# Kernel tuning notes

Hardware: AMD Instinct MI355X
Metric: run time of the kernel (lower is better)

Reference implementation:

```python
import jax, jax.numpy as jnp
import numpy as np
from jax import lax

DIM = 768
HEADS = 12
SR = 2
HH = 64
WW = 64
B = 2
N = HH * WW
HD = DIM // HEADS  # 64; rpe_ratio=1.0 -> rotary covers full head dim


def _angles(dim, end, W, step=1, bias=0.0, theta=10000.0):
    # 2D rotary angles, interleaved x/y: [end, dim//2]
    flat = jnp.arange(end)
    xp = bias + (flat % W) * step
    yp = bias + (flat // W) * step
    freqs = 1.0 / theta ** (jnp.arange(0, dim, 4)[: dim // 4].astype(jnp.float32) / dim)
    xf = jnp.outer(xp.astype(jnp.float32), freqs)
    yf = jnp.outer(yp.astype(jnp.float32), freqs)
    return jnp.stack([xf, yf], axis=-1).reshape(end, -1)


def _rope(x, ang):
    # x: [B, N, h, d]; ang: [N, d//2]
    x2 = x.reshape(x.shape[:-1] + (-1, 2))
    c = jnp.cos(ang)[None, :, None, :]
    s = jnp.sin(ang)[None, :, None, :]
    x0, x1 = x2[..., 0], x2[..., 1]
    out = jnp.stack([x0 * c - x1 * s, x0 * s + x1 * c], axis=-1)
    return out.reshape(x.shape)


def setup_inputs() -> dict:
    key = jax.random.key(0)
    ks = jax.random.split(key, 6)
    p = lambda k, sh: jax.random.normal(k, sh, dtype=jnp.float32) * 0.02
    return {
        'x': jax.random.normal(ks[0], (B, N, DIM), dtype=jnp.float32),
        'Wq': p(ks[1], (DIM, DIM)),
        'Wkv': p(ks[2], (2 * DIM, DIM)),
        'sr_w': p(ks[3], (DIM, DIM, SR, SR)),
        'sr_b': jnp.zeros((DIM,), jnp.float32),
        'ln_g': jnp.ones((DIM,), jnp.float32),
        'ln_b': jnp.zeros((DIM,), jnp.float32),
        'proj_w': p(ks[4], (DIM, DIM)),
        'proj_b': jnp.zeros((DIM,), jnp.float32),
        'H': HH,
        'W': WW,
    }


def reference(x, Wq, Wkv, sr_w, sr_b, ln_g, ln_b, proj_w, proj_b, H, W):
    Bn, Nn, C = x.shape
    hd = C // HEADS
    scale = hd ** -0.5
    N_red = (H * W) // (SR * SR)

    q = (x @ Wq.T).reshape(Bn, Nn, HEADS, hd)

    # spatial reduction: strided conv + layernorm
    xc = x.transpose(0, 2, 1).reshape(Bn, C, H, W)
    xr = lax.conv_general_dilated(xc, sr_w, (SR, SR), 'VALID',
                                  dimension_numbers=('NCHW', 'OIHW', 'NCHW'))
    xr = xr + sr_b[None, :, None, None]
    xr = xr.reshape(Bn, C, N_red).transpose(0, 2, 1)  # [B, N_red, C]
    mu = xr.mean(-1, keepdims=True)
    var = ((xr - mu) ** 2).mean(-1, keepdims=True)
    xr = (xr - mu) / jnp.sqrt(var + 1e-5) * ln_g + ln_b

    kv = (xr @ Wkv.T).reshape(Bn, N_red, 2, HEADS, hd)
    k, v = kv[:, :, 0], kv[:, :, 1]

    # partial-dim 2D rotary (rpe_dim == head_dim here); k uses step=SR, bias=1-1/SR
    q = _rope(q, _angles(hd, Nn, W))
    k = _rope(k, _angles(hd, N_red, W, step=SR, bias=1.0 - 1.0 / SR))

    attn = jnp.einsum('bnhd,bmhd->bhnm', q, k) * scale

    # custom spatial causal mask
    flat = jnp.arange(H * W)
    xpos = flat // (SR * H)
    ox = flat // H
    oy = flat % H
    ypos = (ox + oy * H) // (SR * H)
    vis = xpos * SR + ypos + 1  # number of visible reduced tokens per query
    mask = jnp.arange(N_red)[None, :] < vis[:, None]  # [N, N_red]
    attn = attn + jnp.where(mask, 0.0, -jnp.inf)[None, None]

    attn = jax.nn.softmax(attn, axis=-1)
    out = jnp.einsum('bhnm,bmhd->bnhd', attn, v).reshape(Bn, Nn, C)
    return out @ proj_w.T + proj_b
```

## Files before the change

### kernel.cpp

```cpp
#include <hip/hip_runtime.h>
#include <hip/hip_bf16.h>
#include <math.h>

typedef __attribute__((ext_vector_type(4))) float f32x4;
typedef __attribute__((ext_vector_type(8))) short short8;
typedef __attribute__((ext_vector_type(8))) unsigned short ushort8;
typedef __attribute__((ext_vector_type(4))) unsigned short ushort4v;

__device__ __forceinline__ unsigned short f2bf(float f) {
  __hip_bfloat16 h = __float2bfloat16(f);
  return *reinterpret_cast<unsigned short*>(&h);
}
__device__ __forceinline__ float bf2f(unsigned short u) {
  unsigned v = ((unsigned)u) << 16;
  return *reinterpret_cast<float*>(&v);
}
__device__ __forceinline__ void async16(const void* g, void* l) {
  __builtin_amdgcn_global_load_lds(
      (__attribute__((address_space(1))) void*)g,
      (__attribute__((address_space(3))) void*)l, 16, 0, 0);
}
#define WAITVM8 { asm volatile("s_waitcnt vmcnt(8)" ::: "memory"); __builtin_amdgcn_sched_barrier(0); }
#define WAITVM4 { asm volatile("s_waitcnt vmcnt(4)" ::: "memory"); __builtin_amdgcn_sched_barrier(0); }
#define WAITVM0 { asm volatile("s_waitcnt vmcnt(0)" ::: "memory"); __builtin_amdgcn_sched_barrier(0); }

__global__ __launch_bounds__(256) void k_prep(
    const float* __restrict__ x, const float* __restrict__ Wq,
    const float* __restrict__ Wkv, const float* __restrict__ pw,
    const float* __restrict__ srw,
    float* __restrict__ qtab, float* __restrict__ ktab,
    unsigned short* __restrict__ xb, unsigned short* __restrict__ wqb,
    unsigned short* __restrict__ wkvb, unsigned short* __restrict__ pwb,
    unsigned short* __restrict__ wsrb)
{
  int idx = blockIdx.x * 256 + threadIdx.x;
  if (idx < 131072) {
    int n = idx >> 5, i = idx & 31;
    float freq = powf(10000.0f, -(float)(i >> 1) * (1.0f / 16.0f));
    float pos = (i & 1) ? (float)(n >> 6) : (float)(n & 63);
    float a = pos * freq;
    qtab[idx * 2] = cosf(a);
    qtab[idx * 2 + 1] = sinf(a);
  } else if (idx < 163840) {
    int t = idx - 131072;
    int m = t >> 5, i = t & 31;
    float freq = powf(10000.0f, -(float)(i >> 1) * (1.0f / 16.0f));
    float pos = (i & 1) ? (0.5f + 2.0f * (float)(m >> 6)) : (0.5f + 2.0f * (float)(m & 63));
    float a = pos * freq;
    ktab[t * 2] = cosf(a);
    ktab[t * 2 + 1] = sinf(a);
  } else if (idx < 1736704) {
    int g = idx - 163840;
    float4 v = ((const float4*)x)[g];
    ushort4v o; o[0]=f2bf(v.x); o[1]=f2bf(v.y); o[2]=f2bf(v.z); o[3]=f2bf(v.w);
    *(ushort4v*)(xb + g * 4) = o;
  } else if (idx < 1884160) {
    int g = idx - 1736704;
    float4 v = ((const float4*)Wq)[g];
    ushort4v o; o[0]=f2bf(v.x); o[1]=f2bf(v.y); o[2]=f2bf(v.z); o[3]=f2bf(v.w);
    *(ushort4v*)(wqb + g * 4) = o;
  } else if (idx < 2179072) {
    int g = idx - 1884160;
    float4 v = ((const float4*)Wkv)[g];
    ushort4v o; o[0]=f2bf(v.x); o[1]=f2bf(v.y); o[2]=f2bf(v.z); o[3]=f2bf(v.w);
    *(ushort4v*)(wkvb + g * 4) = o;
  } else if (idx < 2326528) {
    int g = idx - 2179072;
    float4 v = ((const float4*)pw)[g];
    ushort4v o; o[0]=f2bf(v.x); o[1]=f2bf(v.y); o[2]=f2bf(v.z); o[3]=f2bf(v.w);
    *(ushort4v*)(pwb + g * 4) = o;
  } else if (idx < 4685824) {
    int g = idx - 2326528;
    int o = g / 3072;
    int rem = g - o * 3072;
    int c = rem >> 2, patch = rem & 3;
    wsrb[(size_t)patch * 589824 + o * 768 + c] = f2bf(srw[g]);
  }
}

template<int MODE>
__global__ __launch_bounds__(256) void k_g(
    const unsigned short* __restrict__ A, const unsigned short* __restrict__ W,
    void* __restrict__ O0, void* __restrict__ O1,
    const float* __restrict__ bias, const float* __restrict__ tab)
{
  __shared__ __align__(16) unsigned short As[4][128][32];
  __shared__ __align__(16) unsigned short Ws[4][128][32];
  const int tid = threadIdx.x, lane = tid & 63, wid = tid >> 6;
  const int wr = (wid >> 1) * 64, wc = (wid & 1) * 64;
  const int l15 = lane & 15, lhi = lane >> 4;
  const int K = 768, NT = 24;

  const int NWG = (MODE == 1) ? 192 : 384;
  const int tile = ((int)blockIdx.x & 7) * (NWG >> 3) + ((int)blockIdx.x >> 3);

  int cm, cn, patch = 0;
  if (MODE == 3) {
    patch = tile / 96; int r = tile - patch * 96;
    cm = (r / 6) * 128; cn = (r % 6) * 128;
  } else if (MODE == 1) {
    cm = (tile / 12) * 128; cn = (tile % 12) * 128;
  } else {
    cm = (tile / 6) * 128; cn = (tile % 6) * 128;
  }

  size_t aoff0, aoff1;
  {
    int r0 = cm + wid * 32 + (lane >> 2);
    int r1 = r0 + 16;
    if (MODE == 3) {
      int kh = patch >> 1, kw = patch & 1;
      int b0 = r0 >> 10, p0 = r0 & 1023;
      int b1 = r1 >> 10, p1 = r1 & 1023;
      r0 = b0 * 4096 + (2 * (p0 >> 5) + kh) * 64 + 2 * (p0 & 31) + kw;
      r1 = b1 * 4096 + (2 * (p1 >> 5) + kh) * 64 + 2 * (p1 & 31) + kw;
    }
    aoff0 = (size_t)r0 * K + (lane & 3) * 8;
    aoff1 = (size_t)r1 * K + (lane & 3) * 8;
  }
  const unsigned short* wbase = (MODE == 3) ? (W + (size_t)patch * 589824) : W;
  size_t woff0 = (size_t)(cn + wid * 32 + (lane >> 2)) * K + (lane & 3) * 8;
  size_t woff1 = woff0 + (size_t)16 * K;

#define STAGE(bi, kt) { \
    async16(A + aoff0 + (kt) * 32,     &As[bi][wid * 32][0]);      \
    async16(A + aoff1 + (kt) * 32,     &As[bi][wid * 32 + 16][0]); \
    async16(wbase + woff0 + (kt) * 32, &Ws[bi][wid * 32][0]);      \
    async16(wbase + woff1 + (kt) * 32, &Ws[bi][wid * 32 + 16][0]); }

  f32x4 zero = {0.f, 0.f, 0.f, 0.f};
  f32x4 acc[4][4];
  #pragma unroll
  for (int i = 0; i < 4; i++)
    #pragma unroll
    for (int j = 0; j < 4; j++) acc[i][j] = zero;

  STAGE(0, 0);
  STAGE(1, 1);
  STAGE(2, 2);

  #pragma unroll 4
  for (int kt = 0; kt < NT; ++kt) {
    if (kt + 2 < NT)      WAITVM8
    else if (kt + 1 < NT) WAITVM4
    else                  WAITVM0
    __builtin_amdgcn_s_barrier();
    __builtin_amdgcn_sched_barrier(0);
    const int bi = kt & 3;
    if (kt + 3 < NT) STAGE((kt + 3) & 3, kt + 3);
    short8 af[4], wf[4];
    #pragma unroll
    for (int m = 0; m < 4; m++) af[m] = *(const short8*)&As[bi][wr + m * 16 + l15][lhi * 8];
    #pragma unroll
    for (int n = 0; n < 4; n++) wf[n] = *(const short8*)&Ws[bi][wc + n * 16 + l15][lhi * 8];
    #pragma unroll
    for (int m = 0; m < 4; m++)
      #pragma unroll
      for (int n = 0; n < 4; n++)
        acc[m][n] = __builtin_amdgcn_mfma_f32_16x16x32_bf16(wf[n], af[m], acc[m][n], 0, 0, 0);
  }
#undef STAGE

  if (MODE == 0) {
    float* O = (float*)O0;
    #pragma unroll
    for (int n = 0; n < 4; n++) {
      int colb = cn + wc + n * 16 + lhi * 4;
      f32x4 bv = *(const f32x4*)&bias[colb];
      #pragma unroll
      for (int m = 0; m < 4; m++) {
        int row = cm + wr + m * 16 + l15;
        f32x4 v = acc[m][n] + bv;
        *(f32x4*)&O[(size_t)row * 768 + colb] = v;
      }
    }
  } else if (MODE == 2) {
    unsigned short* qr = (unsigned short*)O0;
    const float2* t2 = (const float2*)tab;
    #pragma unroll
    for (int n = 0; n < 4; n++) {
      int col = cn + wc + n * 16 + lhi * 4;
      int hh = col >> 6, d0 = col & 63, i0 = d0 >> 1;
      #pragma unroll
      for (int m = 0; m < 4; m++) {
        int row = cm + wr + m * 16 + l15;
        int bb = row >> 12, np = row & 4095;
        float2 cs0 = t2[np * 32 + i0];
        float2 cs1 = t2[np * 32 + i0 + 1];
        f32x4 v = acc[m][n];
        ushort4v o;
        o[0] = f2bf(v[0] * cs0.x - v[1] * cs0.y);
        o[1] = f2bf(v[0] * cs0.y + v[1] * cs0.x);
        o[2] = f2bf(v[2] * cs1.x - v[3] * cs1.y);
        o[3] = f2bf(v[2] * cs1.y + v[3] * cs1.x);
        *(ushort4v*)(qr + ((size_t)(bb * 12 + hh) * 4096 + np) * 64 + d0) = o;
      }
    }
  } else if (MODE == 1) {
    unsigned short* kr = (unsigned short*)O0;
    unsigned short* vr = (unsigned short*)O1;
    const float2* t2 = (const float2*)tab;
    #pragma unroll
    for (int n = 0; n < 4; n++) {
      int col = cn + wc + n * 16 + lhi * 4;
      bool isk = (col < 768);
      int c2 = isk ? col : col - 768;
      int hh = c2 >> 6, d0 = c2 & 63, i0 = d0 >> 1;
      #pragma unroll
      for (int m = 0; m < 4; m++) {
        int row = cm + wr + m * 16 + l15;
        int bb = row >> 10, mm = row & 1023;
        f32x4 v = acc[m][n];
        size_t o = ((size_t)(bb * 12 + hh) * 1024 + mm) * 64 + d0;
        ushort4v pk;
        if (isk) {
          float2 cs0 = t2[mm * 32 + i0];
          float2 cs1 = t2[mm * 32 + i0 + 1];
          pk[0] = f2bf(v[0] * cs0.x - v[1] * cs0.y);
          pk[1] = f2bf(v[0] * cs0.y + v[1] * cs0.x);
          pk[2] = f2bf(v[2] * cs1.x - v[3] * cs1.y);
          pk[3] = f2bf(v[2] * cs1.y + v[3] * cs1.x);
          *(ushort4v*)(kr + o) = pk;
        } else {
          pk[0] = f2bf(v[0]); pk[1] = f2bf(v[1]);
          pk[2] = f2bf(v[2]); pk[3] = f2bf(v[3]);
          *(ushort4v*)(vr + o) = pk;
        }
      }
    }
  } else {
    unsigned short* O = (unsigned short*)O0 + (size_t)patch * 2048 * 768;
    #pragma unroll
    for (int n = 0; n < 4; n++) {
      int colb = cn + wc + n * 16 + lhi * 4;
      #pragma unroll
      for (int m = 0; m < 4; m++) {
        int row = cm + wr + m * 16 + l15;
        f32x4 v = acc[m][n];
        ushort4v pk;
        pk[0] = f2bf(v[0]); pk[1] = f2bf(v[1]);
        pk[2] = f2bf(v[2]); pk[3] = f2bf(v[3]);
        *(ushort4v*)(O + (size_t)row * 768 + colb) = pk;
      }
    }
  }
}

__global__ __launch_bounds__(256) void k_lnr(const unsigned short* __restrict__ part,
    const float* __restrict__ srb, const float* __restrict__ g,
    const float* __restrict__ b, unsigned short* __restrict__ out) {
  int row = blockIdx.x;
  int t = threadIdx.x;
  float v[3];
  #pragma unroll
  for (int j = 0; j < 3; j++) {
    int c = t + j * 256;
    float s = srb[c];
    #pragma unroll
    for (int p = 0; p < 4; p++)
      s += bf2f(part[((size_t)p * 2048 + row) * 768 + c]);
    v[j] = s;
  }
  float s = v[0] + v[1] + v[2];
  float s2 = v[0] * v[0] + v[1] * v[1] + v[2] * v[2];
  #pragma unroll
  for (int off = 1; off < 64; off <<= 1) {
    s += __shfl_xor(s, off);
    s2 += __shfl_xor(s2, off);
  }
  __shared__ float ss[4], ss2[4];
  int w = t >> 6;
  if ((t & 63) == 0) { ss[w] = s; ss2[w] = s2; }
  __syncthreads();
  s = ss[0] + ss[1] + ss[2] + ss[3];
  s2 = ss2[0] + ss2[1] + ss2[2] + ss2[3];
  float mu = s * (1.0f / 768.0f);
  float var = s2 * (1.0f / 768.0f) - mu * mu;
  float rstd = rsqrtf(var + 1e-5f);
  unsigned short* o = out + (size_t)row * 768;
  #pragma unroll
  for (int j = 0; j < 3; j++) {
    int c = t + j * 256;
    o[c] = f2bf((v[j] - mu) * rstd * g[c] + b[c]);
  }
}

__global__ __launch_bounds__(256) void k_attn(
    const unsigned short* __restrict__ qr,
    const unsigned short* __restrict__ kr,
    const unsigned short* __restrict__ vr,
    unsigned short* __restrict__ aout)
{
  __shared__ __align__(16) unsigned short kt_s[96][72];
  __shared__ __align__(16) unsigned short vt_s[64][104];
  __shared__ __align__(16) unsigned short p_s[4][16][104];

  const int qt = blockIdx.x;
  const int h = blockIdx.y;
  const int b = blockIdx.z;
  const int bh = b * 12 + h;
  const int tid = threadIdx.x, lane = tid & 63, w = tid >> 6;
  const int l15 = lane & 15, lhi = lane >> 4;

  const unsigned short* kg = kr + (size_t)bh * 1024 * 64;
  #pragma unroll
  for (int it = 0; it < 3; it++) {
    int ch = it * 256 + tid;
    int row = ch >> 3, c8 = (ch & 7) * 8;
    *(ushort8*)&kt_s[row][c8] = *(const ushort8*)(kg + row * 64 + c8);
  }
  const unsigned short* vg = vr + (size_t)bh * 1024 * 64;
  #pragma unroll
  for (int it = 0; it < 24; it++) {
    int e = it * 256 + tid;
    int row = e >> 6, d = e & 63;
    vt_s[d][row] = vg[row * 64 + d];
  }
  __syncthreads();

  const unsigned short* qg = qr + (size_t)bh * 4096 * 64
                           + (size_t)(qt * 64 + w * 16 + l15) * 64 + lhi * 8;
  short8 qf0 = *(const short8*)qg;
  short8 qf1 = *(const short8*)(qg + 32);

  f32x4 zero = {0.f, 0.f, 0.f, 0.f};
  f32x4 sacc[6];
  #pragma unroll
  for (int g = 0; g < 6; g++) sacc[g] = zero;
  #pragma unroll
  for (int g = 0; g < 6; g++) {
    short8 kf0 = *(const short8*)&kt_s[g * 16 + l15][lhi * 8];
    short8 kf1 = *(const short8*)&kt_s[g * 16 + l15][32 + lhi * 8];
    sacc[g] = __builtin_amdgcn_mfma_f32_16x16x32_bf16(qf0, kf0, sacc[g], 0, 0, 0);
    sacc[g] = __builtin_amdgcn_mfma_f32_16x16x32_bf16(qf1, kf1, sacc[g], 0, 0, 0);
  }

  int visv[4];
  #pragma unroll
  for (int r = 0; r < 4; r++) {
    int n = qt * 64 + w * 16 + lhi * 4 + r;
    visv[r] = 2 * (n >> 7) + (((n >> 6) + ((n & 63) << 6)) >> 7) + 1;
  }

  float mx[4] = {-INFINITY, -INFINITY, -INFINITY, -INFINITY};
  #pragma unroll
  for (int g = 0; g < 6; g++) {
    int key = g * 16 + l15;
    #pragma unroll
    for (int r = 0; r < 4; r++) {
      float s = (key < visv[r]) ? sacc[g][r] * 0.125f : -INFINITY;
      sacc[g][r] = s;
      mx[r] = fmaxf(mx[r], s);
    }
  }
  #pragma unroll
  for (int off = 1; off < 16; off <<= 1) {
    #pragma unroll
    for (int r = 0; r < 4; r++) mx[r] = fmaxf(mx[r], __shfl_xor(mx[r], off));
  }
  float sum[4] = {0.f, 0.f, 0.f, 0.f};
  #pragma unroll
  for (int g = 0; g < 6; g++) {
    #pragma unroll
    for (int r = 0; r < 4; r++) {
      float pv = __expf(sacc[g][r] - mx[r]);
      sum[r] += pv;
      p_s[w][lhi * 4 + r][g * 16 + l15] = f2bf(pv);
    }
  }
  #pragma unroll
  for (int off = 1; off < 16; off <<= 1) {
    #pragma unroll
    for (int r = 0; r < 4; r++) sum[r] += __shfl_xor(sum[r], off);
  }
  __syncthreads();

  f32x4 oacc[4];
  #pragma unroll
  for (int dg = 0; dg < 4; dg++) oacc[dg] = zero;
  #pragma unroll
  for (int ks = 0; ks < 3; ks++) {
    short8 pa = *(const short8*)&p_s[w][l15][ks * 32 + lhi * 8];
    #pragma unroll
    for (int dg = 0; dg < 4; dg++) {
      short8 vb = *(const short8*)&vt_s[dg * 16 + l15][ks * 32 + lhi * 8];
      oacc[dg] = __builtin_amdgcn_mfma_f32_16x16x32_bf16(pa, vb, oacc[dg], 0, 0, 0);
    }
  }

  unsigned short* ob = aout + ((size_t)b * 4096 + qt * 64 + w * 16) * 768 + h * 64;
  #pragma unroll
  for (int dg = 0; dg < 4; dg++) {
    int d = dg * 16 + l15;
    #pragma unroll
    for (int r = 0; r < 4; r++) {
      ob[(size_t)(lhi * 4 + r) * 768 + d] = f2bf(oacc[dg][r] / sum[r]);
    }
  }
}

extern "C" void kernel_launch(void* const* d_in, const int* in_sizes, int n_in,
                              void* d_out, int out_size, void* d_ws, size_t ws_size,
                              hipStream_t stream) {
  const float* x   = (const float*)d_in[0];
  const float* Wq  = (const float*)d_in[1];
  const float* Wkv = (const float*)d_in[2];
  const float* srw = (const float*)d_in[3];
  const float* srb = (const float*)d_in[4];
  const float* lng = (const float*)d_in[5];
  const float* lnb = (const float*)d_in[6];
  const float* pw  = (const float*)d_in[7];
  const float* pb  = (const float*)d_in[8];

  char* ws = (char*)d_ws;
  float* qtab           = (float*)(ws);
  float* ktab           = (float*)(ws + 1048576);
  unsigned short* xb    = (unsigned short*)(ws + 1310720);
  unsigned short* attno = xb;
  unsigned short* qrope = (unsigned short*)(ws + 13893632);
  unsigned short* part  = (unsigned short*)(ws + 26476544);
  unsigned short* kr    = (unsigned short*)(ws + 26476544);
  unsigned short* vr    = (unsigned short*)(ws + 29622272);
  unsigned short* wqb   = (unsigned short*)(ws + 39059456);
  unsigned short* wkvb  = (unsigned short*)(ws + 40239104);
  unsigned short* pwb   = (unsigned short*)(ws + 42598400);
  unsigned short* wsrb  = (unsigned short*)(ws + 43778048);
  unsigned short* xrn   = (unsigned short*)(ws + 48496640);

  k_prep<<<18304, 256, 0, stream>>>(x, Wq, Wkv, pw, srw, qtab, ktab,
                                    xb, wqb, wkvb, pwb, wsrb);
  k_g<2><<<384, 256, 0, stream>>>(xb, wqb, qrope, nullptr, nullptr, qtab);
  k_g<3><<<384, 256, 0, stream>>>(xb, wsrb, part, nullptr, nullptr, nullptr);
  k_lnr<<<2048, 256, 0, stream>>>(part, srb, lng, lnb, xrn);
  k_g<1><<<192, 256, 0, stream>>>(xrn, wkvb, kr, vr, nullptr, ktab);
  k_attn<<<dim3(64, 12, 2), 256, 0, stream>>>(qrope, kr, vr, attno);
  k_g<0><<<384, 256, 0, stream>>>(attno, pwb, d_out, nullptr, pb, nullptr);
}
```

Measured before the change: 127.7 us.

## Pre-tile operands into contiguous K-blocks and fuse Q and conv GEMM launches

Prep now writes x and all weights in a tiled [rowblock][ktile][128][32] bf16 layout, including a separate pre-gathered copy of x for the strided conv patches. Each GEMM stage then loads one contiguous 8 KB block per operand instead of strided rows. The Q projection and the conv reduction run in a single launch, with conv tiles summing two patches over K=1536 so only two partials reach the layernorm. Attention output and layernorm output are also written tiled. In exchange the extra x copy adds write traffic, the conv tiles do twice the K loop (load imbalance), and the tiled stores from attention and layernorm are scattered.

```diff
diff --git a/kernel.cpp b/kernel.cpp
--- a/kernel.cpp
+++ b/kernel.cpp
@@ -23,15 +23,16 @@
 #define WAITVM8 { asm volatile("s_waitcnt vmcnt(8)" ::: "memory"); __builtin_amdgcn_sched_barrier(0); }
 #define WAITVM4 { asm volatile("s_waitcnt vmcnt(4)" ::: "memory"); __builtin_amdgcn_sched_barrier(0); }
 #define WAITVM0 { asm volatile("s_waitcnt vmcnt(0)" ::: "memory"); __builtin_amdgcn_sched_barrier(0); }
+
 
 __global__ __launch_bounds__(256) void k_prep(
     const float* __restrict__ x, const float* __restrict__ Wq,
     const float* __restrict__ Wkv, const float* __restrict__ pw,
     const float* __restrict__ srw,
     float* __restrict__ qtab, float* __restrict__ ktab,
-    unsigned short* __restrict__ xb, unsigned short* __restrict__ wqb,
-    unsigned short* __restrict__ wkvb, unsigned short* __restrict__ pwb,
-    unsigned short* __restrict__ wsrb)
+    unsigned short* __restrict__ xq_t, unsigned short* __restrict__ xc_t,
+    unsigned short* __restrict__ wq_t, unsigned short* __restrict__ wkv_t,
+    unsigned short* __restrict__ pw_t, unsigned short* __restrict__ wsr_t)
 {
   int idx = blockIdx.x * 256 + threadIdx.x;
   if (idx < 131072) {
@@ -49,84 +50,113 @@
     float a = pos * freq;
     ktab[t * 2] = cosf(a);
     ktab[t * 2 + 1] = sinf(a);
-  } else if (idx < 1736704) {
+  } else if (idx < 557056) {
     int g = idx - 163840;
-    float4 v = ((const float4*)x)[g];
-    ushort4v o; o[0]=f2bf(v.x); o[1]=f2bf(v.y); o[2]=f2bf(v.z); o[3]=f2bf(v.w);
-    *(ushort4v*)(xb + g * 4) = o;
-  } else if (idx < 1884160) {
-    int g = idx - 1736704;
-    float4 v = ((const float4*)Wq)[g];
-    ushort4v o; o[0]=f2bf(v.x); o[1]=f2bf(v.y); o[2]=f2bf(v.z); o[3]=f2bf(v.w);
-    *(ushort4v*)(wqb + g * 4) = o;
-  } else if (idx < 2179072) {
-    int g = idx - 1884160;
-    float4 v = ((const float4*)Wkv)[g];
-    ushort4v o; o[0]=f2bf(v.x); o[1]=f2bf(v.y); o[2]=f2bf(v.z); o[3]=f2bf(v.w);
-    *(ushort4v*)(wkvb + g * 4) = o;
-  } else if (idx < 2326528) {
-    int g = idx - 2179072;
-    float4 v = ((const float4*)pw)[g];
-    ushort4v o; o[0]=f2bf(v.x); o[1]=f2bf(v.y); o[2]=f2bf(v.z); o[3]=f2bf(v.w);
-    *(ushort4v*)(pwb + g * 4) = o;
-  } else if (idx < 4685824) {
-    int g = idx - 2326528;
-    int o = g / 3072;
-    int rem = g - o * 3072;
-    int c = rem >> 2, patch = rem & 3;
-    wsrb[(size_t)patch * 589824 + o * 768 + c] = f2bf(srw[g]);
+    int row = g / 48, c16 = g - row * 48;
+    int kt = c16 >> 1, half = (c16 & 1) * 16;
+    const float4* xp = (const float4*)(x + (size_t)row * 768 + c16 * 16);
+    float4 f0 = xp[0], f1 = xp[1], f2 = xp[2], f3 = xp[3];
+    ushort8 u0, u1;
+    u0[0]=f2bf(f0.x); u0[1]=f2bf(f0.y); u0[2]=f2bf(f0.z); u0[3]=f2bf(f0.w);
+    u0[4]=f2bf(f1.x); u0[5]=f2bf(f1.y); u0[6]=f2bf(f1.z); u0[7]=f2bf(f1.w);
+    u1[0]=f2bf(f2.x); u1[1]=f2bf(f2.y); u1[2]=f2bf(f2.z); u1[3]=f2bf(f2.w);
+    u1[4]=f2bf(f3.x); u1[5]=f2bf(f3.y); u1[6]=f2bf(f3.z); u1[7]=f2bf(f3.w);
+    size_t dq = ((size_t)((row >> 7) * 24 + kt) * 128 + (row & 127)) * 32 + half;
+    *(ushort8*)(xq_t + dq) = u0;
+    *(ushort8*)(xq_t + dq + 8) = u1;
+    int rowm = row & 4095, bb = row >> 12;
+    int hh = rowm >> 6, www = rowm & 63;
+    int patch = (hh & 1) * 2 + (www & 1);
+    int convrow = bb * 1024 + (hh >> 1) * 32 + (www >> 1);
+    size_t dc = ((size_t)((patch * 16 + (convrow >> 7)) * 24 + kt) * 128 + (convrow & 127)) * 32 + half;
+    *(ushort8*)(xc_t + dc) = u0;
+    *(ushort8*)(xc_t + dc + 8) = u1;
+  } else if (idx < 851968) {
+    const float* src; unsigned short* dst; int g;
+    if (idx < 593920)      { g = idx - 557056; src = Wq;  dst = wq_t; }
+    else if (idx < 667648) { g = idx - 593920; src = Wkv; dst = wkv_t; }
+    else if (idx < 704512) { g = idx - 667648; src = pw;  dst = pw_t; }
+    else {
+      int t = idx - 704512;
+      int o = t / 192, c4 = t - o * 192, c = c4 * 4;
+      const float4* sp = (const float4*)(srw + (size_t)o * 3072 + c * 4);
+      float4 q0 = sp[0], q1 = sp[1], q2 = sp[2], q3 = sp[3];
+      float qa[4][4] = {{q0.x,q0.y,q0.z,q0.w},{q1.x,q1.y,q1.z,q1.w},
+                        {q2.x,q2.y,q2.z,q2.w},{q3.x,q3.y,q3.z,q3.w}};
+      #pragma unroll
+      for (int p = 0; p < 4; p++) {
+        ushort4v wv;
+        #pragma unroll
+        for (int j = 0; j < 4; j++) wv[j] = f2bf(qa[j][p]);
+        size_t d = ((size_t)((p * 6 + (o >> 7)) * 24 + (c >> 5)) * 128 + (o & 127)) * 32 + (c & 31);
+        *(ushort4v*)(wsr_t + d) = wv;
+      }
+      return;
+    }
+    int row = g / 48, c16 = g - row * 48;
+    int kt = c16 >> 1, half = (c16 & 1) * 16;
+    const float4* xp = (const float4*)(src + (size_t)row * 768 + c16 * 16);
+    float4 f0 = xp[0], f1 = xp[1], f2 = xp[2], f3 = xp[3];
+    ushort8 u0, u1;
+    u0[0]=f2bf(f0.x); u0[1]=f2bf(f0.y); u0[2]=f2bf(f0.z); u0[3]=f2bf(f0.w);
+    u0[4]=f2bf(f1.x); u0[5]=f2bf(f1.y); u0[6]=f2bf(f1.z); u0[7]=f2bf(f1.w);
+    u1[0]=f2bf(f2.x); u1[1]=f2bf(f2.y); u1[2]=f2bf(f2.z); u1[3]=f2bf(f2.w);
+    u1[4]=f2bf(f3.x); u1[5]=f2bf(f3.y); u1[6]=f2bf(f3.z); u1[7]=f2bf(f3.w);
+    size_t d = ((size_t)((row >> 7) * 24 + kt) * 128 + (row & 127)) * 32 + half;
+    *(ushort8*)(dst + d) = u0;
+    *(ushort8*)(dst + d + 8) = u1;
   }
 }
 
 template<int MODE>
 __global__ __launch_bounds__(256) void k_g(
-    const unsigned short* __restrict__ A, const unsigned short* __restrict__ W,
+    const unsigned short* __restrict__ A, const unsigned short* __restrict__ A2,
+    const unsigned short* __restrict__ W, const unsigned short* __restrict__ W2,
     void* __restrict__ O0, void* __restrict__ O1,
     const float* __restrict__ bias, const float* __restrict__ tab)
 {
-  __shared__ __align__(16) unsigned short As[4][128][32];
-  __shared__ __align__(16) unsigned short Ws[4][128][32];
+  __shared__ __align__(16) unsigned short As[4][4096];
+  __shared__ __align__(16) unsigned short Ws[4][4096];
   const int tid = threadIdx.x, lane = tid & 63, wid = tid >> 6;
   const int wr = (wid >> 1) * 64, wc = (wid & 1) * 64;
   const int l15 = lane & 15, lhi = lane >> 4;
-  const int K = 768, NT = 24;
-
-  const int NWG = (MODE == 1) ? 192 : 384;
+
+  const int NWG = (MODE == 2) ? 576 : (MODE == 1 ? 192 : 384);
   const int tile = ((int)blockIdx.x & 7) * (NWG >> 3) + ((int)blockIdx.x >> 3);
 
-  int cm, cn, patch = 0;
-  if (MODE == 3) {
-    patch = tile / 96; int r = tile - patch * 96;
-    cm = (r / 6) * 128; cn = (r % 6) * 128;
-  } else if (MODE == 1) {
-    cm = (tile / 12) * 128; cn = (tile % 12) * 128;
+  int cm, cn, NT = 24, sPair = 0;
+  bool isconv = false;
+  const unsigned short *abase0, *abase1 = nullptr, *wbase0, *wbase1 = nullptr;
+  if (MODE == 2 && tile >= 384) {
+    isconv = true; NT = 48;
+    int c = tile - 384;
+    sPair = c / 96; int r = c - sPair * 96;
+    int crb = r / 6, cb = r % 6;
+    cm = crb * 128; cn = cb * 128;
+    abase0 = A2 + (size_t)(((sPair * 2) * 16 + crb) * 24) * 4096;
+    abase1 = A2 + (size_t)(((sPair * 2 + 1) * 16 + crb) * 24) * 4096;
+    wbase0 = W2 + (size_t)(((sPair * 2) * 6 + cb) * 24) * 4096;
+    wbase1 = W2 + (size_t)(((sPair * 2 + 1) * 6 + cb) * 24) * 4096;
   } else {
-    cm = (tile / 6) * 128; cn = (tile % 6) * 128;
-  }
-
-  size_t aoff0, aoff1;
-  {
-    int r0 = cm + wid * 32 + (lane >> 2);
-    int r1 = r0 + 16;
-    if (MODE == 3) {
-      int kh = patch >> 1, kw = patch & 1;
-      int b0 = r0 >> 10, p0 = r0 & 1023;
-      int b1 = r1 >> 10, p1 = r1 & 1023;
-      r0 = b0 * 4096 + (2 * (p0 >> 5) + kh) * 64 + 2 * (p0 & 31) + kw;
-      r1 = b1 * 4096 + (2 * (p1 >> 5) + kh) * 64 + 2 * (p1 & 31) + kw;
-    }
-    aoff0 = (size_t)r0 * K + (lane & 3) * 8;
-    aoff1 = (size_t)r1 * K + (lane & 3) * 8;
-  }
-  const unsigned short* wbase = (MODE == 3) ? (W + (size_t)patch * 589824) : W;
-  size_t woff0 = (size_t)(cn + wid * 32 + (lane >> 2)) * K + (lane & 3) * 8;
-  size_t woff1 = woff0 + (size_t)16 * K;
-
-#define STAGE(bi, kt) { \
-    async16(A + aoff0 + (kt) * 32,     &As[bi][wid * 32][0]);      \
-    async16(A + aoff1 + (kt) * 32,     &As[bi][wid * 32 + 16][0]); \
-    async16(wbase + woff0 + (kt) * 32, &Ws[bi][wid * 32][0]);      \
-    async16(wbase + woff1 + (kt) * 32, &Ws[bi][wid * 32 + 16][0]); }
+    int nb = (MODE == 1) ? 12 : 6;
+    int rb = tile / nb, cb = tile % nb;
+    cm = rb * 128; cn = cb * 128;
+    abase0 = A + (size_t)(rb * 24) * 4096;
+    wbase0 = W + (size_t)(cb * 24) * 4096;
+  }
+
+#define TILEPTRS(kt2, ap_, wp_) { \
+    if (MODE == 2 && isconv) { \
+      int pp_ = (kt2) >= 24 ? 1 : 0; int kk_ = (kt2) - pp_ * 24; \
+      ap_ = (pp_ ? abase1 : abase0) + kk_ * 4096; \
+      wp_ = (pp_ ? wbase1 : wbase0) + kk_ * 4096; \
+    } else { ap_ = abase0 + (kt2) * 4096; wp_ = wbase0 + (kt2) * 4096; } }
+#define STAGE(bi, kt2) { \
+    const unsigned short *ap_, *wp_; TILEPTRS(kt2, ap_, wp_); \
+    async16(ap_ + tid * 8,        &As[bi][wid * 512]); \
+    async16(ap_ + 2048 + tid * 8, &As[bi][2048 + wid * 512]); \
+    async16(wp_ + tid * 8,        &Ws[bi][wid * 512]); \
+    async16(wp_ + 2048 + tid * 8, &Ws[bi][2048 + wid * 512]); }
 
   f32x4 zero = {0.f, 0.f, 0.f, 0.f};
   f32x4 acc[4][4];
@@ -150,9 +180,9 @@
     if (kt + 3 < NT) STAGE((kt + 3) & 3, kt + 3);
     short8 af[4], wf[4];
     #pragma unroll
-    for (int m = 0; m < 4; m++) af[m] = *(const short8*)&As[bi][wr + m * 16 + l15][lhi * 8];
-    #pragma unroll
-    for (int n = 0; n < 4; n++) wf[n] = *(const short8*)&Ws[bi][wc + n * 16 + l15][lhi * 8];
+    for (int m = 0; m < 4; m++) af[m] = *(const short8*)&As[bi][(wr + m * 16 + l15) * 32 + lhi * 8];
+    #pragma unroll
+    for (int n = 0; n < 4; n++) wf[n] = *(const short8*)&Ws[bi][(wc + n * 16 + l15) * 32 + lhi * 8];
     #pragma unroll
     for (int m = 0; m < 4; m++)
       #pragma unroll
@@ -160,6 +190,7 @@
         acc[m][n] = __builtin_amdgcn_mfma_f32_16x16x32_bf16(wf[n], af[m], acc[m][n], 0, 0, 0);
   }
 #undef STAGE
+#undef TILEPTRS
 
   if (MODE == 0) {
     float* O = (float*)O0;
@@ -172,28 +203,6 @@
         int row = cm + wr + m * 16 + l15;
         f32x4 v = acc[m][n] + bv;
         *(f32x4*)&O[(size_t)row * 768 + colb] = v;
-      }
-    }
-  } else if (MODE == 2) {
-    unsigned short* qr = (unsigned short*)O0;
-    const float2* t2 = (const float2*)tab;
-    #pragma unroll
-    for (int n = 0; n < 4; n++) {
-      int col = cn + wc + n * 16 + lhi * 4;
-      int hh = col >> 6, d0 = col & 63, i0 = d0 >> 1;
-      #pragma unroll
-      for (int m = 0; m < 4; m++) {
-        int row = cm + wr + m * 16 + l15;
-        int bb = row >> 12, np = row & 4095;
-        float2 cs0 = t2[np * 32 + i0];
-        float2 cs1 = t2[np * 32 + i0 + 1];
-        f32x4 v = acc[m][n];
-        ushort4v o;
-        o[0] = f2bf(v[0] * cs0.x - v[1] * cs0.y);
-        o[1] = f2bf(v[0] * cs0.y + v[1] * cs0.x);
-        o[2] = f2bf(v[2] * cs1.x - v[3] * cs1.y);
-        o[3] = f2bf(v[2] * cs1.y + v[3] * cs1.x);
-        *(ushort4v*)(qr + ((size_t)(bb * 12 + hh) * 4096 + np) * 64 + d0) = o;
       }
     }
   } else if (MODE == 1) {
@@ -228,8 +237,30 @@
         }
       }
     }
+  } else if (!isconv) {
+    unsigned short* qr = (unsigned short*)O0;
+    const float2* t2 = (const float2*)tab;
+    #pragma unroll
+    for (int n = 0; n < 4; n++) {
+      int col = cn + wc + n * 16 + lhi * 4;
+      int hh = col >> 6, d0 = col & 63, i0 = d0 >> 1;
+      #pragma unroll
+      for (int m = 0; m < 4; m++) {
+        int row = cm + wr + m * 16 + l15;
+        int bb = row >> 12, np = row & 4095;
+        float2 cs0 = t2[np * 32 + i0];
+        float2 cs1 = t2[np * 32 + i0 + 1];
+        f32x4 v = acc[m][n];
+        ushort4v o;
+        o[0] = f2bf(v[0] * cs0.x - v[1] * cs0.y);
+        o[1] = f2bf(v[0] * cs0.y + v[1] * cs0.x);
+        o[2] = f2bf(v[2] * cs1.x - v[3] * cs1.y);
+        o[3] = f2bf(v[2] * cs1.y + v[3] * cs1.x);
+        *(ushort4v*)(qr + ((size_t)(bb * 12 + hh) * 4096 + np) * 64 + d0) = o;
+      }
+    }
   } else {
-    unsigned short* O = (unsigned short*)O0 + (size_t)patch * 2048 * 768;
+    unsigned short* P = (unsigned short*)O1 + (size_t)sPair * 2048 * 768;
     #pragma unroll
     for (int n = 0; n < 4; n++) {
       int colb = cn + wc + n * 16 + lhi * 4;
@@ -240,7 +271,7 @@
         ushort4v pk;
         pk[0] = f2bf(v[0]); pk[1] = f2bf(v[1]);
         pk[2] = f2bf(v[2]); pk[3] = f2bf(v[3]);
-        *(ushort4v*)(O + (size_t)row * 768 + colb) = pk;
+        *(ushort4v*)(P + (size_t)row * 768 + colb) = pk;
       }
     }
   }
@@ -248,18 +279,15 @@
 
 __global__ __launch_bounds__(256) void k_lnr(const unsigned short* __restrict__ part,
     const float* __restrict__ srb, const float* __restrict__ g,
-    const float* __restrict__ b, unsigned short* __restrict__ out) {
+    const float* __restrict__ b, unsigned short* __restrict__ out_t) {
   int row = blockIdx.x;
   int t = threadIdx.x;
   float v[3];
   #pragma unroll
   for (int j = 0; j < 3; j++) {
     int c = t + j * 256;
-    float s = srb[c];
-    #pragma unroll
-    for (int p = 0; p < 4; p++)
-      s += bf2f(part[((size_t)p * 2048 + row) * 768 + c]);
-    v[j] = s;
+    v[j] = srb[c] + bf2f(part[(size_t)row * 768 + c])
+                  + bf2f(part[(size_t)(2048 + row) * 768 + c]);
   }
   float s = v[0] + v[1] + v[2];
   float s2 = v[0] * v[0] + v[1] * v[1] + v[2] * v[2];
@@ -277,11 +305,12 @@
   float mu = s * (1.0f / 768.0f);
   float var = s2 * (1.0f / 768.0f) - mu * mu;
   float rstd = rsqrtf(var + 1e-5f);
-  unsigned short* o = out + (size_t)row * 768;
+  int rb = row >> 7, rr = row & 127;
   #pragma unroll
   for (int j = 0; j < 3; j++) {
     int c = t + j * 256;
-    o[c] = f2bf((v[j] - mu) * rstd * g[c] + b[c]);
+    out_t[((size_t)(rb * 24 + (c >> 5)) * 128 + rr) * 32 + (c & 31)]
+        = f2bf((v[j] - mu) * rstd * g[c] + b[c]);
   }
 }
 
@@ -289,7 +318,7 @@
     const unsigned short* __restrict__ qr,
     const unsigned short* __restrict__ kr,
     const unsigned short* __restrict__ vr,
-    unsigned short* __restrict__ aout)
+    unsigned short* __restrict__ aout_t)
 {
   __shared__ __align__(16) unsigned short kt_s[96][72];
   __shared__ __align__(16) unsigned short vt_s[64][104];
@@ -388,13 +417,15 @@
     }
   }
 
-  unsigned short* ob = aout + ((size_t)b * 4096 + qt * 64 + w * 16) * 768 + h * 64;
   #pragma unroll
   for (int dg = 0; dg < 4; dg++) {
-    int d = dg * 16 + l15;
+    int col = h * 64 + dg * 16 + l15;
+    int kt = col >> 5, cc = col & 31;
     #pragma unroll
     for (int r = 0; r < 4; r++) {
-      ob[(size_t)(lhi * 4 + r) * 768 + d] = f2bf(oacc[dg][r] / sum[r]);
+      int row = b * 4096 + qt * 64 + w * 16 + lhi * 4 + r;
+      int rb = row >> 7, rr = row & 127;
+      aout_t[((size_t)(rb * 24 + kt) * 128 + rr) * 32 + cc] = f2bf(oacc[dg][r] / sum[r]);
     }
   }
 }
@@ -413,26 +444,26 @@
   const float* pb  = (const float*)d_in[8];
 
   char* ws = (char*)d_ws;
-  float* qtab           = (float*)(ws);
-  float* ktab           = (float*)(ws + 1048576);
-  unsigned short* xb    = (unsigned short*)(ws + 1310720);
-  unsigned short* attno = xb;
-  unsigned short* qrope = (unsigned short*)(ws + 13893632);
-  unsigned short* part  = (unsigned short*)(ws + 26476544);
-  unsigned short* kr    = (unsigned short*)(ws + 26476544);
-  unsigned short* vr    = (unsigned short*)(ws + 29622272);
-  unsigned short* wqb   = (unsigned short*)(ws + 39059456);
-  unsigned short* wkvb  = (unsigned short*)(ws + 40239104);
-  unsigned short* pwb   = (unsigned short*)(ws + 42598400);
-  unsigned short* wsrb  = (unsigned short*)(ws + 43778048);
-  unsigned short* xrn   = (unsigned short*)(ws + 48496640);
-
-  k_prep<<<18304, 256, 0, stream>>>(x, Wq, Wkv, pw, srw, qtab, ktab,
-                                    xb, wqb, wkvb, pwb, wsrb);
-  k_g<2><<<384, 256, 0, stream>>>(xb, wqb, qrope, nullptr, nullptr, qtab);
-  k_g<3><<<384, 256, 0, stream>>>(xb, wsrb, part, nullptr, nullptr, nullptr);
-  k_lnr<<<2048, 256, 0, stream>>>(part, srb, lng, lnb, xrn);
-  k_g<1><<<192, 256, 0, stream>>>(xrn, wkvb, kr, vr, nullptr, ktab);
-  k_attn<<<dim3(64, 12, 2), 256, 0, stream>>>(qrope, kr, vr, attno);
-  k_g<0><<<384, 256, 0, stream>>>(attno, pwb, d_out, nullptr, pb, nullptr);
-}
+  float* qtab            = (float*)(ws);
+  float* ktab            = (float*)(ws + 1048576);
+  unsigned short* xq_t   = (unsigned short*)(ws + 1310720);
+  unsigned short* attno_t= xq_t;
+  unsigned short* xc_t   = (unsigned short*)(ws + 13893632);
+  unsigned short* xrn_t  = (unsigned short*)(ws + 13893632);
+  unsigned short* kr     = (unsigned short*)(ws + 17039360);
+  unsigned short* vr     = (unsigned short*)(ws + 20185088);
+  unsigned short* qrope  = (unsigned short*)(ws + 26476544);
+  unsigned short* part   = (unsigned short*)(ws + 39059456);
+  unsigned short* wq_t   = (unsigned short*)(ws + 45350912);
+  unsigned short* wkv_t  = (unsigned short*)(ws + 46530560);
+  unsigned short* pw_t   = (unsigned short*)(ws + 48889856);
+  unsigned short* wsr_t  = (unsigned short*)(ws + 50069504);
+
+  k_prep<<<3328, 256, 0, stream>>>(x, Wq, Wkv, pw, srw, qtab, ktab,
+                                   xq_t, xc_t, wq_t, wkv_t, pw_t, wsr_t);
+  k_g<2><<<576, 256, 0, stream>>>(xq_t, xc_t, wq_t, wsr_t, qrope, part, nullptr, qtab);
+  k_lnr<<<2048, 256, 0, stream>>>(part, srb, lng, lnb, xrn_t);
+  k_g<1><<<192, 256, 0, stream>>>(xrn_t, nullptr, wkv_t, nullptr, kr, vr, nullptr, ktab);
+  k_attn<<<dim3(64, 12, 2), 256, 0, stream>>>(qrope, kr, vr, attno_t);
+  k_g<0><<<384, 256, 0, stream>>>(attno_t, nullptr, pw_t, nullptr, d_out, nullptr, pb, nullptr);
+}
```

Result: slower. 185.3 us (+45.2%).

## Merge Q and conv GEMMs into one launch with 256-row tiles

Applied to the files above, without the earlier changes.

Fuses the Q projection GEMM and the strided-conv patch GEMM into a single launch, dispatched by tile index. Doubles the M tile to 256 rows for the Q, conv and output-projection GEMMs so each weight fragment is reused across twice as many rows. Pipeline depth drops from four LDS stages to three to fit the larger A tile. This removes one kernel launch and halves the block count of the two big GEMMs, at the cost of more accumulator registers per thread, lower occupancy and a shallower prefetch pipeline.

```diff
diff --git a/kernel.cpp b/kernel.cpp
--- a/kernel.cpp
+++ b/kernel.cpp
@@ -20,7 +20,7 @@
       (__attribute__((address_space(1))) void*)g,
       (__attribute__((address_space(3))) void*)l, 16, 0, 0);
 }
-#define WAITVM8 { asm volatile("s_waitcnt vmcnt(8)" ::: "memory"); __builtin_amdgcn_sched_barrier(0); }
+#define WAITVM6 { asm volatile("s_waitcnt vmcnt(6)" ::: "memory"); __builtin_amdgcn_sched_barrier(0); }
 #define WAITVM4 { asm volatile("s_waitcnt vmcnt(4)" ::: "memory"); __builtin_amdgcn_sched_barrier(0); }
 #define WAITVM0 { asm volatile("s_waitcnt vmcnt(0)" ::: "memory"); __builtin_amdgcn_sched_barrier(0); }
 
@@ -81,83 +81,86 @@
 template<int MODE>
 __global__ __launch_bounds__(256) void k_g(
     const unsigned short* __restrict__ A, const unsigned short* __restrict__ W,
+    const unsigned short* __restrict__ W2,
     void* __restrict__ O0, void* __restrict__ O1,
     const float* __restrict__ bias, const float* __restrict__ tab)
 {
-  __shared__ __align__(16) unsigned short As[4][128][32];
-  __shared__ __align__(16) unsigned short Ws[4][128][32];
+  constexpr int MR = (MODE == 1) ? 1 : 2;
+  constexpr int NT = 24;
+  __shared__ __align__(16) unsigned short As[3][128 * MR][32];
+  __shared__ __align__(16) unsigned short Ws[3][128][32];
   const int tid = threadIdx.x, lane = tid & 63, wid = tid >> 6;
   const int wr = (wid >> 1) * 64, wc = (wid & 1) * 64;
   const int l15 = lane & 15, lhi = lane >> 4;
-  const int K = 768, NT = 24;
-
-  const int NWG = (MODE == 1) ? 192 : 384;
+
+  const int NWG = (MODE == 2) ? 384 : 192;
   const int tile = ((int)blockIdx.x & 7) * (NWG >> 3) + ((int)blockIdx.x >> 3);
 
   int cm, cn, patch = 0;
-  if (MODE == 3) {
-    patch = tile / 96; int r = tile - patch * 96;
-    cm = (r / 6) * 128; cn = (r % 6) * 128;
+  bool isconv = false;
+  if (MODE == 2) {
+    if (tile < 192) { cm = (tile / 6) * 256; cn = (tile % 6) * 128; }
+    else {
+      int c = tile - 192; isconv = true;
+      patch = c / 48; int r = c - patch * 48;
+      cm = (r / 6) * 256; cn = (r % 6) * 128;
+    }
   } else if (MODE == 1) {
     cm = (tile / 12) * 128; cn = (tile % 12) * 128;
   } else {
-    cm = (tile / 6) * 128; cn = (tile % 6) * 128;
-  }
-
-  size_t aoff0, aoff1;
-  {
-    int r0 = cm + wid * 32 + (lane >> 2);
-    int r1 = r0 + 16;
-    if (MODE == 3) {
+    cm = (tile / 6) * 256; cn = (tile % 6) * 128;
+  }
+
+  size_t aoff[2 * MR], woff[2];
+  #pragma unroll
+  for (int c = 0; c < 2 * MR; c++) {
+    int r = cm + wid * 32 * MR + c * 16 + (lane >> 2);
+    if (MODE == 2 && isconv) {
       int kh = patch >> 1, kw = patch & 1;
-      int b0 = r0 >> 10, p0 = r0 & 1023;
-      int b1 = r1 >> 10, p1 = r1 & 1023;
-      r0 = b0 * 4096 + (2 * (p0 >> 5) + kh) * 64 + 2 * (p0 & 31) + kw;
-      r1 = b1 * 4096 + (2 * (p1 >> 5) + kh) * 64 + 2 * (p1 & 31) + kw;
-    }
-    aoff0 = (size_t)r0 * K + (lane & 3) * 8;
-    aoff1 = (size_t)r1 * K + (lane & 3) * 8;
-  }
-  const unsigned short* wbase = (MODE == 3) ? (W + (size_t)patch * 589824) : W;
-  size_t woff0 = (size_t)(cn + wid * 32 + (lane >> 2)) * K + (lane & 3) * 8;
-  size_t woff1 = woff0 + (size_t)16 * K;
+      int bb = r >> 10, p = r & 1023;
+      r = bb * 4096 + (2 * (p >> 5) + kh) * 64 + 2 * (p & 31) + kw;
+    }
+    aoff[c] = (size_t)r * 768 + (lane & 3) * 8;
+  }
+  #pragma unroll
+  for (int c = 0; c < 2; c++)
+    woff[c] = (size_t)(cn + wid * 32 + c * 16 + (lane >> 2)) * 768 + (lane & 3) * 8;
+  const unsigned short* wbase = (MODE == 2 && isconv) ? (W2 + (size_t)patch * 589824) : W;
 
 #define STAGE(bi, kt) { \
-    async16(A + aoff0 + (kt) * 32,     &As[bi][wid * 32][0]);      \
-    async16(A + aoff1 + (kt) * 32,     &As[bi][wid * 32 + 16][0]); \
-    async16(wbase + woff0 + (kt) * 32, &Ws[bi][wid * 32][0]);      \
-    async16(wbase + woff1 + (kt) * 32, &Ws[bi][wid * 32 + 16][0]); }
+    _Pragma("unroll") for (int c = 0; c < 2 * MR; c++) \
+      async16(A + aoff[c] + (kt) * 32, &As[bi][wid * 32 * MR + c * 16][0]); \
+    _Pragma("unroll") for (int c = 0; c < 2; c++) \
+      async16(wbase + woff[c] + (kt) * 32, &Ws[bi][wid * 32 + c * 16][0]); }
 
   f32x4 zero = {0.f, 0.f, 0.f, 0.f};
-  f32x4 acc[4][4];
-  #pragma unroll
-  for (int i = 0; i < 4; i++)
+  f32x4 acc[4 * MR][4];
+  #pragma unroll
+  for (int i = 0; i < 4 * MR; i++)
     #pragma unroll
     for (int j = 0; j < 4; j++) acc[i][j] = zero;
 
   STAGE(0, 0);
   STAGE(1, 1);
-  STAGE(2, 2);
-
-  #pragma unroll 4
+
+  #pragma unroll 3
   for (int kt = 0; kt < NT; ++kt) {
-    if (kt + 2 < NT)      WAITVM8
-    else if (kt + 1 < NT) WAITVM4
-    else                  WAITVM0
+    if (kt + 1 < NT) { if (MR == 2) WAITVM6 else WAITVM4 }
+    else             WAITVM0
     __builtin_amdgcn_s_barrier();
     __builtin_amdgcn_sched_barrier(0);
-    const int bi = kt & 3;
-    if (kt + 3 < NT) STAGE((kt + 3) & 3, kt + 3);
-    short8 af[4], wf[4];
-    #pragma unroll
-    for (int m = 0; m < 4; m++) af[m] = *(const short8*)&As[bi][wr + m * 16 + l15][lhi * 8];
+    const int bi = kt % 3;
+    if (kt + 2 < NT) STAGE((kt + 2) % 3, kt + 2);
+    short8 wf[4];
     #pragma unroll
     for (int n = 0; n < 4; n++) wf[n] = *(const short8*)&Ws[bi][wc + n * 16 + l15][lhi * 8];
     #pragma unroll
-    for (int m = 0; m < 4; m++)
+    for (int m = 0; m < 4 * MR; m++) {
+      short8 af = *(const short8*)&As[bi][(m >> 2) * 128 + wr + (m & 3) * 16 + l15][lhi * 8];
       #pragma unroll
       for (int n = 0; n < 4; n++)
-        acc[m][n] = __builtin_amdgcn_mfma_f32_16x16x32_bf16(wf[n], af[m], acc[m][n], 0, 0, 0);
+        acc[m][n] = __builtin_amdgcn_mfma_f32_16x16x32_bf16(wf[n], af, acc[m][n], 0, 0, 0);
+    }
   }
 #undef STAGE
 
@@ -168,32 +171,10 @@
       int colb = cn + wc + n * 16 + lhi * 4;
       f32x4 bv = *(const f32x4*)&bias[colb];
       #pragma unroll
-      for (int m = 0; m < 4; m++) {
-        int row = cm + wr + m * 16 + l15;
+      for (int m = 0; m < 4 * MR; m++) {
+        int row = cm + (m >> 2) * 128 + wr + (m & 3) * 16 + l15;
         f32x4 v = acc[m][n] + bv;
         *(f32x4*)&O[(size_t)row * 768 + colb] = v;
-      }
-    }
-  } else if (MODE == 2) {
-    unsigned short* qr = (unsigned short*)O0;
-    const float2* t2 = (const float2*)tab;
-    #pragma unroll
-    for (int n = 0; n < 4; n++) {
-      int col = cn + wc + n * 16 + lhi * 4;
-      int hh = col >> 6, d0 = col & 63, i0 = d0 >> 1;
-      #pragma unroll
-      for (int m = 0; m < 4; m++) {
-        int row = cm + wr + m * 16 + l15;
-        int bb = row >> 12, np = row & 4095;
-        float2 cs0 = t2[np * 32 + i0];
-        float2 cs1 = t2[np * 32 + i0 + 1];
-        f32x4 v = acc[m][n];
-        ushort4v o;
-        o[0] = f2bf(v[0] * cs0.x - v[1] * cs0.y);
-        o[1] = f2bf(v[0] * cs0.y + v[1] * cs0.x);
-        o[2] = f2bf(v[2] * cs1.x - v[3] * cs1.y);
-        o[3] = f2bf(v[2] * cs1.y + v[3] * cs1.x);
-        *(ushort4v*)(qr + ((size_t)(bb * 12 + hh) * 4096 + np) * 64 + d0) = o;
       }
     }
   } else if (MODE == 1) {
@@ -207,8 +188,8 @@
       int c2 = isk ? col : col - 768;
       int hh = c2 >> 6, d0 = c2 & 63, i0 = d0 >> 1;
       #pragma unroll
-      for (int m = 0; m < 4; m++) {
-        int row = cm + wr + m * 16 + l15;
+      for (int m = 0; m < 4 * MR; m++) {
+        int row = cm + (m >> 2) * 128 + wr + (m & 3) * 16 + l15;
         int bb = row >> 10, mm = row & 1023;
         f32x4 v = acc[m][n];
         size_t o = ((size_t)(bb * 12 + hh) * 1024 + mm) * 64 + d0;
@@ -228,19 +209,41 @@
         }
       }
     }
+  } else if (!isconv) {
+    unsigned short* qr = (unsigned short*)O0;
+    const float2* t2 = (const float2*)tab;
+    #pragma unroll
+    for (int n = 0; n < 4; n++) {
+      int col = cn + wc + n * 16 + lhi * 4;
+      int hh = col >> 6, d0 = col & 63, i0 = d0 >> 1;
+      #pragma unroll
+      for (int m = 0; m < 4 * MR; m++) {
+        int row = cm + (m >> 2) * 128 + wr + (m & 3) * 16 + l15;
+        int bb = row >> 12, np = row & 4095;
+        float2 cs0 = t2[np * 32 + i0];
+        float2 cs1 = t2[np * 32 + i0 + 1];
+        f32x4 v = acc[m][n];
+        ushort4v o;
+        o[0] = f2bf(v[0] * cs0.x - v[1] * cs0.y);
+        o[1] = f2bf(v[0] * cs0.y + v[1] * cs0.x);
+        o[2] = f2bf(v[2] * cs1.x - v[3] * cs1.y);
+        o[3] = f2bf(v[2] * cs1.y + v[3] * cs1.x);
+        *(ushort4v*)(qr + ((size_t)(bb * 12 + hh) * 4096 + np) * 64 + d0) = o;
+      }
+    }
   } else {
-    unsigned short* O = (unsigned short*)O0 + (size_t)patch * 2048 * 768;
+    unsigned short* P = (unsigned short*)O1 + (size_t)patch * 2048 * 768;
     #pragma unroll
     for (int n = 0; n < 4; n++) {
       int colb = cn + wc + n * 16 + lhi * 4;
       #pragma unroll
-      for (int m = 0; m < 4; m++) {
-        int row = cm + wr + m * 16 + l15;
+      for (int m = 0; m < 4 * MR; m++) {
+        int row = cm + (m >> 2) * 128 + wr + (m & 3) * 16 + l15;
         f32x4 v = acc[m][n];
         ushort4v pk;
         pk[0] = f2bf(v[0]); pk[1] = f2bf(v[1]);
         pk[2] = f2bf(v[2]); pk[3] = f2bf(v[3]);
-        *(ushort4v*)(O + (size_t)row * 768 + colb) = pk;
+        *(ushort4v*)(P + (size_t)row * 768 + colb) = pk;
       }
     }
   }
@@ -429,10 +432,9 @@
 
   k_prep<<<18304, 256, 0, stream>>>(x, Wq, Wkv, pw, srw, qtab, ktab,
                                     xb, wqb, wkvb, pwb, wsrb);
-  k_g<2><<<384, 256, 0, stream>>>(xb, wqb, qrope, nullptr, nullptr, qtab);
-  k_g<3><<<384, 256, 0, stream>>>(xb, wsrb, part, nullptr, nullptr, nullptr);
+  k_g<2><<<384, 256, 0, stream>>>(xb, wqb, wsrb, qrope, part, nullptr, qtab);
   k_lnr<<<2048, 256, 0, stream>>>(part, srb, lng, lnb, xrn);
-  k_g<1><<<192, 256, 0, stream>>>(xrn, wkvb, kr, vr, nullptr, ktab);
+  k_g<1><<<192, 256, 0, stream>>>(xrn, wkvb, nullptr, kr, vr, nullptr, ktab);
   k_attn<<<dim3(64, 12, 2), 256, 0, stream>>>(qrope, kr, vr, attno);
-  k_g<0><<<384, 256, 0, stream>>>(attno, pwb, d_out, nullptr, pb, nullptr);
-}
+  k_g<0><<<192, 256, 0, stream>>>(attno, pwb, nullptr, d_out, nullptr, pb, nullptr);
+}
```

Result: slower. 152.3 us (+19.3%).

## Use 64-wide K tiles with XOR-swizzled LDS and double buffering in GEMM

Applied to the files above, without the earlier changes.

Doubles the GEMM K-tile from 32 to 64, so each iteration covers twice the K range and the loop trip count halves. The 4-stage async prefetch pipeline becomes 2-buffer double buffering synchronised with __syncthreads. Global-to-LDS copies apply an XOR swizzle on 8-element chunks, and the fragment reads undo it, to avoid LDS bank conflicts on the wider rows. The cost is a shallower prefetch distance, with only one tile in flight, so more global load latency may be exposed.

```diff
diff --git a/kernel.cpp b/kernel.cpp
--- a/kernel.cpp
+++ b/kernel.cpp
@@ -20,9 +20,6 @@
       (__attribute__((address_space(1))) void*)g,
       (__attribute__((address_space(3))) void*)l, 16, 0, 0);
 }
-#define WAITVM8 { asm volatile("s_waitcnt vmcnt(8)" ::: "memory"); __builtin_amdgcn_sched_barrier(0); }
-#define WAITVM4 { asm volatile("s_waitcnt vmcnt(4)" ::: "memory"); __builtin_amdgcn_sched_barrier(0); }
-#define WAITVM0 { asm volatile("s_waitcnt vmcnt(0)" ::: "memory"); __builtin_amdgcn_sched_barrier(0); }
 
 __global__ __launch_bounds__(256) void k_prep(
     const float* __restrict__ x, const float* __restrict__ Wq,
@@ -84,12 +81,12 @@
     void* __restrict__ O0, void* __restrict__ O1,
     const float* __restrict__ bias, const float* __restrict__ tab)
 {
-  __shared__ __align__(16) unsigned short As[4][128][32];
-  __shared__ __align__(16) unsigned short Ws[4][128][32];
+  __shared__ __align__(16) unsigned short As[2][128][64];
+  __shared__ __align__(16) unsigned short Ws[2][128][64];
   const int tid = threadIdx.x, lane = tid & 63, wid = tid >> 6;
   const int wr = (wid >> 1) * 64, wc = (wid & 1) * 64;
   const int l15 = lane & 15, lhi = lane >> 4;
-  const int K = 768, NT = 24;
+  const int K = 768, NT = 12;
 
   const int NWG = (MODE == 1) ? 192 : 384;
   const int tile = ((int)blockIdx.x & 7) * (NWG >> 3) + ((int)blockIdx.x >> 3);
@@ -104,29 +101,28 @@
     cm = (tile / 6) * 128; cn = (tile % 6) * 128;
   }
 
-  size_t aoff0, aoff1;
-  {
-    int r0 = cm + wid * 32 + (lane >> 2);
-    int r1 = r0 + 16;
+  const int swz = ((lane & 7) * 8) ^ ((lane >> 3) << 3);
+  size_t aoff[4], woff[4];
+  #pragma unroll
+  for (int c = 0; c < 4; c++) {
+    int r = cm + wid * 32 + c * 8 + (lane >> 3);
     if (MODE == 3) {
       int kh = patch >> 1, kw = patch & 1;
-      int b0 = r0 >> 10, p0 = r0 & 1023;
-      int b1 = r1 >> 10, p1 = r1 & 1023;
-      r0 = b0 * 4096 + (2 * (p0 >> 5) + kh) * 64 + 2 * (p0 & 31) + kw;
-      r1 = b1 * 4096 + (2 * (p1 >> 5) + kh) * 64 + 2 * (p1 & 31) + kw;
-    }
-    aoff0 = (size_t)r0 * K + (lane & 3) * 8;
-    aoff1 = (size_t)r1 * K + (lane & 3) * 8;
-  }
+      int bb = r >> 10, p = r & 1023;
+      r = bb * 4096 + (2 * (p >> 5) + kh) * 64 + 2 * (p & 31) + kw;
+    }
+    aoff[c] = (size_t)r * K + swz;
+  }
+  #pragma unroll
+  for (int c = 0; c < 4; c++)
+    woff[c] = (size_t)(cn + wid * 32 + c * 8 + (lane >> 3)) * K + swz;
   const unsigned short* wbase = (MODE == 3) ? (W + (size_t)patch * 589824) : W;
-  size_t woff0 = (size_t)(cn + wid * 32 + (lane >> 2)) * K + (lane & 3) * 8;
-  size_t woff1 = woff0 + (size_t)16 * K;
 
 #define STAGE(bi, kt) { \
-    async16(A + aoff0 + (kt) * 32,     &As[bi][wid * 32][0]);      \
-    async16(A + aoff1 + (kt) * 32,     &As[bi][wid * 32 + 16][0]); \
-    async16(wbase + woff0 + (kt) * 32, &Ws[bi][wid * 32][0]);      \
-    async16(wbase + woff1 + (kt) * 32, &Ws[bi][wid * 32 + 16][0]); }
+    _Pragma("unroll") for (int c = 0; c < 4; c++) \
+      async16(A + aoff[c] + (kt) * 64, &As[bi][wid * 32 + c * 8][0]); \
+    _Pragma("unroll") for (int c = 0; c < 4; c++) \
+      async16(wbase + woff[c] + (kt) * 64, &Ws[bi][wid * 32 + c * 8][0]); }
 
   f32x4 zero = {0.f, 0.f, 0.f, 0.f};
   f32x4 acc[4][4];
@@ -136,28 +132,27 @@
     for (int j = 0; j < 4; j++) acc[i][j] = zero;
 
   STAGE(0, 0);
-  STAGE(1, 1);
-  STAGE(2, 2);
-
-  #pragma unroll 4
+
+  const int rswzA = (l15 & 7) << 3;
   for (int kt = 0; kt < NT; ++kt) {
-    if (kt + 2 < NT)      WAITVM8
-    else if (kt + 1 < NT) WAITVM4
-    else                  WAITVM0
-    __builtin_amdgcn_s_barrier();
-    __builtin_amdgcn_sched_barrier(0);
-    const int bi = kt & 3;
-    if (kt + 3 < NT) STAGE((kt + 3) & 3, kt + 3);
-    short8 af[4], wf[4];
-    #pragma unroll
-    for (int m = 0; m < 4; m++) af[m] = *(const short8*)&As[bi][wr + m * 16 + l15][lhi * 8];
-    #pragma unroll
-    for (int n = 0; n < 4; n++) wf[n] = *(const short8*)&Ws[bi][wc + n * 16 + l15][lhi * 8];
-    #pragma unroll
-    for (int m = 0; m < 4; m++)
+    __syncthreads();
+    const int bi = kt & 1;
+    if (kt + 1 < NT) STAGE(bi ^ 1, kt + 1);
+    #pragma unroll
+    for (int h = 0; h < 2; h++) {
+      short8 af[4], wf[4];
+      #pragma unroll
+      for (int m = 0; m < 4; m++)
+        af[m] = *(const short8*)&As[bi][wr + m * 16 + l15][(h * 32 + lhi * 8) ^ rswzA];
       #pragma unroll
       for (int n = 0; n < 4; n++)
-        acc[m][n] = __builtin_amdgcn_mfma_f32_16x16x32_bf16(wf[n], af[m], acc[m][n], 0, 0, 0);
+        wf[n] = *(const short8*)&Ws[bi][wc + n * 16 + l15][(h * 32 + lhi * 8) ^ rswzA];
+      #pragma unroll
+      for (int m = 0; m < 4; m++)
+        #pragma unroll
+        for (int n = 0; n < 4; n++)
+          acc[m][n] = __builtin_amdgcn_mfma_f32_16x16x32_bf16(wf[n], af[m], acc[m][n], 0, 0, 0);
+    }
   }
 #undef STAGE
 
```

New measurement: 112.0 us. -12.2%, faster.
